# Kernel optimization log

Measured on AMD Instinct MI355X. Metric: run time of the kernel, lower is better.

The kernel has to match this reference:

```python
import jax, jax.numpy as jnp
import numpy as np

DIM = 3072
NUM_HEADS = 24
HEAD_DIM = 128
INNER = NUM_HEADS * HEAD_DIM
EPS = 1e-5


def _layernorm(x, eps=EPS):
    # affine-free LayerNorm over the last (head_dim) axis
    mu = jnp.mean(x, axis=-1, keepdims=True)
    var = jnp.mean(jnp.square(x - mu), axis=-1, keepdims=True)
    return (x - mu) * jax.lax.rsqrt(var + eps)


def _rope_interleaved(x, cos, sin):
    # x: (B, S_img, H, D); cos/sin: (S_img, D//2). Non-neox (interleaved) style.
    x1 = x[..., 0::2]
    x2 = x[..., 1::2]
    c = cos[None, :, None, :]
    s = sin[None, :, None, :]
    o1 = x1 * c - x2 * s
    o2 = x2 * c + x1 * s
    return jnp.stack([o1, o2], axis=-1).reshape(x.shape)


def setup_inputs() -> dict:
    key = jax.random.key(0)
    ks = jax.random.split(key, 8)
    B, S_txt, S_img = 1, 256, 2048
    hidden_states = jax.random.normal(ks[0], (B, S_img, DIM), dtype=jnp.float32)
    encoder_hidden_states = jax.random.normal(ks[1], (B, S_txt, DIM), dtype=jnp.float32)
    cos = jax.random.uniform(ks[2], (S_img, HEAD_DIM // 2), dtype=jnp.float32)
    sin = jax.random.uniform(ks[3], (S_img, HEAD_DIM // 2), dtype=jnp.float32)
    Wqkv = jax.random.normal(ks[4], (DIM, 3 * INNER), dtype=jnp.float32) * (DIM ** -0.5)
    bqkv = jnp.zeros((3 * INNER,), dtype=jnp.float32)
    Wout = jax.random.normal(ks[5], (INNER, DIM), dtype=jnp.float32) * (INNER ** -0.5)
    bout = jnp.zeros((DIM,), dtype=jnp.float32)
    return {
        "hidden_states": hidden_states,
        "encoder_hidden_states": encoder_hidden_states,
        "cos": cos,
        "sin": sin,
        "Wqkv": Wqkv,
        "bqkv": bqkv,
        "Wout": Wout,
        "bout": bout,
        "text_seq_length": 256,
    }


def reference(hidden_states, encoder_hidden_states, cos, sin, Wqkv, bqkv, Wout, bout, text_seq_length):
    T = text_seq_length
    x = jnp.concatenate([encoder_hidden_states, hidden_states], axis=1)  # (B, S, dim)
    B, S, _ = x.shape
    qkv = x @ Wqkv + bqkv  # (B, S, 3*inner)
    q, k, v = jnp.split(qkv, 3, axis=-1)
    q = q.reshape(B, S, NUM_HEADS, HEAD_DIM)
    k = k.reshape(B, S, NUM_HEADS, HEAD_DIM)
    v = v.reshape(B, S, NUM_HEADS, HEAD_DIM)
    q = _layernorm(q)
    k = _layernorm(k)
    # partial RoPE: only on image-token slice
    q = jnp.concatenate([q[:, :T], _rope_interleaved(q[:, T:], cos, sin)], axis=1)
    k = jnp.concatenate([k[:, :T], _rope_interleaved(k[:, T:], cos, sin)], axis=1)
    scale = 1.0 / (HEAD_DIM ** 0.5)
    scores = jnp.einsum("bqhd,bkhd->bhqk", q, k) * scale
    probs = jax.nn.softmax(scores, axis=-1)
    out = jnp.einsum("bhqk,bkhd->bqhd", probs, v)
    out = out.reshape(B, S, INNER)
    out = out @ Wout + bout
    encoder_out = out[:, :T, :]
    hidden_out = out[:, T:, :]
    return (hidden_out, encoder_out)
```

## Files before the change

### kernel.cpp

```cpp
#include <hip/hip_runtime.h>

#define DIMC 3072
#define NH 24
#define HD 128
#define QKV_N 9216
#define S_TXT 256
#define S_IMG 2048
#define S_TOT 2304

typedef _Float16 f16x8 __attribute__((ext_vector_type(8)));
typedef _Float16 f16x4 __attribute__((ext_vector_type(4)));
typedef _Float16 f16x2 __attribute__((ext_vector_type(2)));
typedef float f32x4 __attribute__((ext_vector_type(4)));

#define MFMA(A, B, C) __builtin_amdgcn_mfma_f32_16x16x32_f16(A, B, C, 0, 0, 0)

#define QSCALE (0.08838834764831845f * 1.4426950408889634f)

__device__ __forceinline__ void gl2lds16(const _Float16* g, _Float16* l) {
    __builtin_amdgcn_global_load_lds(
        (const __attribute__((address_space(1))) unsigned int*)g,
        (__attribute__((address_space(3))) unsigned int*)l,
        16, 0, 0);
}

__global__ __launch_bounds__(256) void prep(
    const float* __restrict__ enc, const float* __restrict__ hid,
    const float* __restrict__ Wqkv, const float* __restrict__ Wout,
    _Float16* __restrict__ xh, _Float16* __restrict__ Wth,
    _Float16* __restrict__ W2h)
{
    __shared__ float T[64][68];
    const int bid = blockIdx.x;
    const int t = threadIdx.x;

    if (bid < S_TOT) {
        const int s = bid;
        const float* src = (s < S_TXT) ? enc + (size_t)s * DIMC
                                       : hid + (size_t)(s - S_TXT) * DIMC;
#pragma unroll
        for (int it = 0; it < 3; ++it) {
            const int i = (it * 256 + t) * 4;
            float4 v = *(const float4*)(src + i);
            f16x4 hv;
            hv.x = (_Float16)v.x; hv.y = (_Float16)v.y;
            hv.z = (_Float16)v.z; hv.w = (_Float16)v.w;
            *(f16x4*)(xh + (size_t)s * DIMC + i) = hv;
        }
        return;
    }

    const float* W;
    _Float16* Th;
    int n0, k0, ldw;
    if (bid < S_TOT + 144 * 48) {
        const int b2 = bid - S_TOT;
        W = Wqkv; Th = Wth; ldw = QKV_N;
        n0 = (b2 % 144) * 64; k0 = (b2 / 144) * 64;
    } else {
        const int b2 = bid - S_TOT - 144 * 48;
        W = Wout; Th = W2h; ldw = DIMC;
        n0 = (b2 % 48) * 64; k0 = (b2 / 48) * 64;
    }
    {
        const int r = t >> 2, c4 = (t & 3) * 16;
#pragma unroll
        for (int j = 0; j < 4; ++j) {
            float4 v = *(const float4*)(W + (size_t)(k0 + r) * ldw + n0 + c4 + j * 4);
            *(float4*)&T[r][c4 + j * 4] = v;
        }
    }
    __syncthreads();
    const int nr = t >> 2, kp = (t & 3) * 16;
    f16x8 hv0, hv1;
#pragma unroll
    for (int j = 0; j < 8; ++j) hv0[j] = (_Float16)T[kp + j][nr];
#pragma unroll
    for (int j = 0; j < 8; ++j) hv1[j] = (_Float16)T[kp + 8 + j][nr];
    _Float16* dh = Th + (size_t)(n0 + nr) * DIMC + k0 + kp;
    *(f16x8*)(dh) = hv0; *(f16x8*)(dh + 8) = hv1;
}

#define GEMM_DB_PRE()                                                         \
    const int cpx = (int)gridDim.x >> 3;                                      \
    const int wgid = (blockIdx.x & 7) * cpx + (blockIdx.x >> 3);              \
    const int bm = (wgid % 18) * 128;                                         \
    const int bn = (wgid / 18) * 128;                                         \
    const int tid = threadIdx.x;                                              \
    const int l = tid & 63, w = tid >> 6;                                     \
    const int wr = w >> 1, wc = w & 1;                                        \
    const int lr = l & 15, g = l >> 4;                                        \
    const int row0 = w * 16 + (l >> 2);                                       \
    const int swz = (((l & 3) ^ ((row0 >> 1) & 3)) * 8);                      \
    const _Float16* gA0 = Ah + (size_t)(bm + row0) * DIMC + swz;              \
    const _Float16* gA1 = Ah + (size_t)(bm + 64 + row0) * DIMC + swz;         \
    const _Float16* gB0 = Bh + (size_t)(bn + row0) * DIMC + swz;              \
    const _Float16* gB1 = Bh + (size_t)(bn + 64 + row0) * DIMC + swz;         \
    int aoff[4], boff[4];                                                     \
    _Pragma("unroll")                                                         \
    for (int i = 0; i < 4; ++i) {                                             \
        const int ra = wr * 64 + i * 16 + lr;                                 \
        const int rb = wc * 64 + i * 16 + lr;                                 \
        aoff[i] = ra * 32 + ((g ^ ((ra >> 1) & 3)) * 8);                      \
        boff[i] = rb * 32 + ((g ^ ((rb >> 1) & 3)) * 8);                      \
    }

#define GEMM_STAGE(dd, k0) do {                                               \
    gl2lds16(gA0 + (k0), &Ash[dd][(w * 16) * 32]);                            \
    gl2lds16(gA1 + (k0), &Ash[dd][(64 + w * 16) * 32]);                       \
    gl2lds16(gB0 + (k0), &Bsh[dd][(w * 16) * 32]);                            \
    gl2lds16(gB1 + (k0), &Bsh[dd][(64 + w * 16) * 32]);                       \
} while (0)

#define GEMM_DB_LOOP()                                                        \
    f32x4 acc[4][4] = {};                                                     \
    GEMM_STAGE(0, 0);                                                         \
    __syncthreads();                                                          \
    for (int T = 0; T < DIMC / 32; ++T) {                                     \
        const int d = T & 1;                                                  \
        if (T + 1 < DIMC / 32) GEMM_STAGE(d ^ 1, (T + 1) * 32);               \
        f16x8 bhf[4];                                                         \
        _Pragma("unroll")                                                     \
        for (int ni = 0; ni < 4; ++ni)                                        \
            bhf[ni] = *(const f16x8*)&Bsh[d][boff[ni]];                       \
        __builtin_amdgcn_s_setprio(1);                                        \
        _Pragma("unroll")                                                     \
        for (int mi = 0; mi < 4; ++mi) {                                      \
            f16x8 ahf = *(const f16x8*)&Ash[d][aoff[mi]];                     \
            _Pragma("unroll")                                                 \
            for (int ni = 0; ni < 4; ++ni)                                    \
                acc[mi][ni] = MFMA(ahf, bhf[ni], acc[mi][ni]);                \
        }                                                                     \
        __builtin_amdgcn_s_setprio(0);                                        \
        __syncthreads();                                                      \
    }

__global__ __launch_bounds__(256) void gemm_qkv(
    const _Float16* __restrict__ Ah, const _Float16* __restrict__ Bh,
    const float* __restrict__ bias,
    _Float16* __restrict__ Qh, _Float16* __restrict__ Kh,
    _Float16* __restrict__ Vt)
{
    __shared__ __attribute__((aligned(16))) _Float16 Ash[2][128 * 32];
    __shared__ __attribute__((aligned(16))) _Float16 Bsh[2][128 * 32];
    GEMM_DB_PRE()
    GEMM_DB_LOOP()

    const int nb = bn >> 7;
    const int typ = nb / NH;
    const int h = nb % NH;

    if (typ == 2) {
#pragma unroll
        for (int mi = 0; mi < 4; ++mi) {
            const int sbase = bm + wr * 64 + mi * 16 + g * 4;
#pragma unroll
            for (int ni = 0; ni < 4; ++ni) {
                const int col = wc * 64 + ni * 16 + lr;
                const float bv = bias[bn + col];
                f16x4 vv;
                vv.x = (_Float16)(acc[mi][ni][0] + bv);
                vv.y = (_Float16)(acc[mi][ni][1] + bv);
                vv.z = (_Float16)(acc[mi][ni][2] + bv);
                vv.w = (_Float16)(acc[mi][ni][3] + bv);
                *(f16x4*)&Vt[((size_t)h * HD + col) * S_TOT + sbase] = vv;
            }
        }
    } else {
        _Float16* dst = (typ ? Kh : Qh) + (size_t)h * S_TOT * HD;
#pragma unroll
        for (int mi = 0; mi < 4; ++mi)
#pragma unroll
            for (int ni = 0; ni < 4; ++ni) {
                const int col = wc * 64 + ni * 16 + lr;
                const float bv = bias[bn + col];
#pragma unroll
                for (int e = 0; e < 4; ++e) {
                    const int r = bm + wr * 64 + mi * 16 + g * 4 + e;
                    dst[(size_t)r * HD + col] = (_Float16)(acc[mi][ni][e] + bv);
                }
            }
    }
}

__global__ __launch_bounds__(256) void gemm_out(
    const _Float16* __restrict__ Ah, const _Float16* __restrict__ Bh,
    const float* __restrict__ bias, float* __restrict__ C)
{
    __shared__ __attribute__((aligned(16))) _Float16 Ash[2][128 * 32];
    __shared__ __attribute__((aligned(16))) _Float16 Bsh[2][128 * 32];
    GEMM_DB_PRE()
    GEMM_DB_LOOP()

#pragma unroll
    for (int mi = 0; mi < 4; ++mi)
#pragma unroll
        for (int ni = 0; ni < 4; ++ni) {
            const int cl = bn + wc * 64 + ni * 16 + lr;
            const float bv = bias[cl];
#pragma unroll
            for (int e = 0; e < 4; ++e) {
                const int r = bm + wr * 64 + mi * 16 + g * 4 + e;
                const int gr = (r < S_TXT) ? (S_IMG + r) : (r - S_TXT);
                C[(size_t)gr * DIMC + cl] = acc[mi][ni][e] + bv;
            }
        }
}

__global__ __launch_bounds__(256) void ln_rope_inplace(
    _Float16* __restrict__ Qh, _Float16* __restrict__ Kh,
    const float* __restrict__ cost, const float* __restrict__ sint)
{
    const int wave = threadIdx.x >> 6;
    const int lane = threadIdx.x & 63;
    const int task = blockIdx.x * 4 + wave;
    const int s = task / 48;
    const int rem = task % 48;
    const int qk = rem / 24;
    const int h = rem % 24;

    _Float16* p = (qk ? Kh : Qh) + ((size_t)h * S_TOT + s) * HD + lane * 2;
    f16x2 xv = *(const f16x2*)p;
    float x0 = (float)xv.x, x1 = (float)xv.y;

    float sum = x0 + x1;
    float sq = x0 * x0 + x1 * x1;
#pragma unroll
    for (int off = 1; off < 64; off <<= 1) {
        sum += __shfl_xor(sum, off, 64);
        sq  += __shfl_xor(sq, off, 64);
    }
    const float mu = sum * (1.0f / 128.0f);
    const float var = sq * (1.0f / 128.0f) - mu * mu;
    const float rstd = rsqrtf(var + 1e-5f);
    float y0 = (x0 - mu) * rstd;
    float y1 = (x1 - mu) * rstd;

    if (s >= S_TXT) {
        const int ip = s - S_TXT;
        const float c = cost[ip * 64 + lane];
        const float sn = sint[ip * 64 + lane];
        const float o0 = y0 * c - y1 * sn;
        const float o1 = y1 * c + y0 * sn;
        y0 = o0; y1 = o1;
    }
    if (qk == 0) { y0 *= QSCALE; y1 *= QSCALE; }

    f16x2 hv; hv.x = (_Float16)y0; hv.y = (_Float16)y1;
    *(f16x2*)p = hv;
}

__global__ __launch_bounds__(512) void attn_mfma(
    const _Float16* __restrict__ Qg, const _Float16* __restrict__ Kg,
    const _Float16* __restrict__ Vg, _Float16* __restrict__ aoh)
{
    __shared__ __attribute__((aligned(16))) _Float16 Ksh[4 * 64 * 32];
    __shared__ __attribute__((aligned(16))) _Float16 Vsh[128 * 64];
    __shared__ __attribute__((aligned(16))) _Float16 Pah[8 * 16 * 64];

    const int wgid = ((int)blockIdx.x & 7) * 54 + ((int)blockIdx.x >> 3);
    const int h = wgid / 18;
    const int q0 = (wgid % 18) * 128;
    const int tid = threadIdx.x;
    const int w = tid >> 6, l = tid & 63;
    const int lr = l & 15, g = l >> 4;

    const int qrow = q0 + w * 16 + lr;
    const _Float16* qb = Qg + ((size_t)h * S_TOT + qrow) * HD + g * 8;
    f16x8 qh[4];
#pragma unroll
    for (int db = 0; db < 4; ++db)
        qh[db] = *(const f16x8*)(qb + db * 32);

    f32x4 o[8] = {};
    float mrow = -3.0e38f, lrow = 0.0f;

    const int kxr = (lr >> 1) & 3;
    const int px  = lr & 7;
    int ksl[4];
#pragma unroll
    for (int db = 0; db < 4; ++db) ksl[db] = (g ^ kxr ^ db) * 8;
    const int vs0 = (g ^ px) * 8;
    const int vs1 = ((4 + g) ^ px) * 8;

    const int kkv = tid >> 3, kd = tid & 7;
    const int kdb = kd >> 1, kg0 = (kd & 1) * 2;
    const int kx = (kkv >> 1) & 3;
    const int kbase = kdb * 2048 + kkv * 32;
    const int vd = tid >> 2, vh = tid & 3;
    const int vx = vd & 7;
    const int vbase = vd * 64;
    const int vg0 = vh * 2;
    const _Float16* gK = Kg + ((size_t)h * S_TOT + kkv) * HD + kd * 16;
    const _Float16* gV = Vg + ((size_t)h * HD + vd) * S_TOT + vh * 16;

    uint4 rK0, rK1, rV0, rV1;
#define LOADKV(kv0) { \
    rK0 = *(const uint4*)(gK + (size_t)(kv0) * HD);     rK1 = *(const uint4*)(gK + (size_t)(kv0) * HD + 8); \
    rV0 = *(const uint4*)(gV + (kv0));                  rV1 = *(const uint4*)(gV + (kv0) + 8); }

    LOADKV(0);

    for (int kb = 0; kb < S_TOT / 64; ++kb) {
        __syncthreads();
        *(uint4*)&Ksh[kbase + (((kg0 + 0) ^ kx ^ kdb) * 8)] = rK0;
        *(uint4*)&Ksh[kbase + (((kg0 + 1) ^ kx ^ kdb) * 8)] = rK1;
        *(uint4*)&Vsh[vbase + (((vg0 + 0) ^ vx) * 8)] = rV0;
        *(uint4*)&Vsh[vbase + (((vg0 + 1) ^ vx) * 8)] = rV1;
        __syncthreads();
        if (kb + 1 < S_TOT / 64) LOADKV((kb + 1) * 64);

        f32x4 sT[4] = {};
        __builtin_amdgcn_s_setprio(1);
#pragma unroll
        for (int db = 0; db < 4; ++db)
#pragma unroll
            for (int mf = 0; mf < 4; ++mf) {
                f16x8 kf = *(const f16x8*)&Ksh[db * 2048 + (mf * 16 + lr) * 32 + ksl[db]];
                sT[mf] = MFMA(kf, qh[db], sT[mf]);
            }
        __builtin_amdgcn_s_setprio(0);

        float pm = -3.0e38f;
#pragma unroll
        for (int mf = 0; mf < 4; ++mf)
#pragma unroll
            for (int e = 0; e < 4; ++e)
                pm = fmaxf(pm, sT[mf][e]);
        pm = fmaxf(pm, __shfl_xor(pm, 16, 64));
        pm = fmaxf(pm, __shfl_xor(pm, 32, 64));

        if (__any(pm > mrow + 11.0f)) {
            const float mnew = fmaxf(mrow, pm);
            const float alpha = exp2f(mrow - mnew);
            lrow *= alpha;
            mrow = mnew;
            const float a0 = __shfl(alpha, g * 4 + 0, 64);
            const float a1 = __shfl(alpha, g * 4 + 1, 64);
            const float a2 = __shfl(alpha, g * 4 + 2, 64);
            const float a3 = __shfl(alpha, g * 4 + 3, 64);
#pragma unroll
            for (int df = 0; df < 8; ++df) {
                o[df][0] *= a0; o[df][1] *= a1; o[df][2] *= a2; o[df][3] *= a3;
            }
        }

        float rs = 0.0f;
        float ex_[4][4];
#pragma unroll
        for (int mf = 0; mf < 4; ++mf)
#pragma unroll
            for (int e = 0; e < 4; ++e) {
                const float pv = exp2f(sT[mf][e] - mrow);
                ex_[mf][e] = pv;
                rs += pv;
            }
        rs += __shfl_xor(rs, 16, 64);
        rs += __shfl_xor(rs, 32, 64);
        lrow += rs;

        {
            const int pbase = w * 1024 + lr * 64;
#pragma unroll
            for (int mf = 0; mf < 4; ++mf) {
                const int slot = ((mf * 2 + (g >> 1)) ^ px) * 8 + (g & 1) * 4;
                f16x2 t0; t0.x = (_Float16)ex_[mf][0]; t0.y = (_Float16)ex_[mf][1];
                f16x2 t1; t1.x = (_Float16)ex_[mf][2]; t1.y = (_Float16)ex_[mf][3];
                *(f16x2*)&Pah[pbase + slot]     = t0;
                *(f16x2*)&Pah[pbase + slot + 2] = t1;
            }
        }

        f16x8 pa0 = *(const f16x8*)&Pah[w * 1024 + lr * 64 + vs0];
        f16x8 pa1 = *(const f16x8*)&Pah[w * 1024 + lr * 64 + vs1];
        __builtin_amdgcn_s_setprio(1);
#pragma unroll
        for (int df = 0; df < 8; ++df) {
            f16x8 vf0 = *(const f16x8*)&Vsh[(df * 16 + lr) * 64 + vs0];
            f16x8 vf1 = *(const f16x8*)&Vsh[(df * 16 + lr) * 64 + vs1];
            o[df] = MFMA(pa0, vf0, o[df]);
            o[df] = MFMA(pa1, vf1, o[df]);
        }
        __builtin_amdgcn_s_setprio(0);
    }
#undef LOADKV

    const float inv = 1.0f / lrow;
    const float b0 = __shfl(inv, g * 4 + 0, 64);
    const float b1 = __shfl(inv, g * 4 + 1, 64);
    const float b2 = __shfl(inv, g * 4 + 2, 64);
    const float b3 = __shfl(inv, g * 4 + 3, 64);
    const float bb[4] = {b0, b1, b2, b3};
#pragma unroll
    for (int df = 0; df < 8; ++df)
#pragma unroll
        for (int e = 0; e < 4; ++e) {
            const int r = q0 + w * 16 + g * 4 + e;
            aoh[(size_t)r * DIMC + h * HD + df * 16 + lr] = (_Float16)(o[df][e] * bb[e]);
        }
}

extern "C" void kernel_launch(void* const* d_in, const int* in_sizes, int n_in,
                              void* d_out, int out_size, void* d_ws, size_t ws_size,
                              hipStream_t stream)
{
    const float* hid  = (const float*)d_in[0];
    const float* enc  = (const float*)d_in[1];
    const float* cost = (const float*)d_in[2];
    const float* sint = (const float*)d_in[3];
    const float* Wqkv = (const float*)d_in[4];
    const float* bqkv = (const float*)d_in[5];
    const float* Wout = (const float*)d_in[6];
    const float* bout = (const float*)d_in[7];
    float* out = (float*)d_out;

    char* ws = (char*)d_ws;
    _Float16* Qh  = (_Float16*)(ws + 0);
    _Float16* Kh  = (_Float16*)(ws + 14155776);
    _Float16* Vth = (_Float16*)(ws + 28311552);
    _Float16* aoh = (_Float16*)(ws + 42467328);
    _Float16* xh  = (_Float16*)(ws + 56623104);
    _Float16* Wth = (_Float16*)(ws + 70778880);
    _Float16* W2h = (_Float16*)(ws + 127401984);

    prep<<<S_TOT + 144 * 48 + 48 * 48, 256, 0, stream>>>(
        enc, hid, Wqkv, Wout, xh, Wth, W2h);
    gemm_qkv<<<18 * 72, 256, 0, stream>>>(xh, Wth, bqkv, Qh, Kh, Vth);
    ln_rope_inplace<<<(S_TOT * 48) / 4, 256, 0, stream>>>(Qh, Kh, cost, sint);
    attn_mfma<<<432, 512, 0, stream>>>(Qh, Kh, Vth, aoh);
    gemm_out<<<18 * 24, 256, 0, stream>>>(aoh, W2h, bout, out);
}
```

Baseline: 457.4 us.

## Single-buffer GEMM LDS staging and give each attention wave two query tiles

The GEMM kernels drop the double-buffered LDS pipeline and the setprio hints. They now load each K-slice synchronously and sync before compute, with the per-wave load rows remapped. The attention kernel halves its block size to 4 waves, and each wave processes 32 query rows as two 16-row tiles. This reuses every K/V fragment read from LDS across two MFMA streams and halves the waves contending for the K/V tiles. The cost is higher register pressure and lost load/compute overlap in the GEMMs, which risks stalls on global-to-LDS latency.

```diff
diff --git a/kernel.cpp b/kernel.cpp
--- a/kernel.cpp
+++ b/kernel.cpp
@@ -81,7 +81,7 @@
     *(f16x8*)(dh) = hv0; *(f16x8*)(dh + 8) = hv1;
 }
 
-#define GEMM_DB_PRE()                                                         \
+#define GEMM_PRE()                                                            \
     const int cpx = (int)gridDim.x >> 3;                                      \
     const int wgid = (blockIdx.x & 7) * cpx + (blockIdx.x >> 3);              \
     const int bm = (wgid % 18) * 128;                                         \
@@ -90,12 +90,18 @@
     const int l = tid & 63, w = tid >> 6;                                     \
     const int wr = w >> 1, wc = w & 1;                                        \
     const int lr = l & 15, g = l >> 4;                                        \
-    const int row0 = w * 16 + (l >> 2);                                       \
-    const int swz = (((l & 3) ^ ((row0 >> 1) & 3)) * 8);                      \
-    const _Float16* gA0 = Ah + (size_t)(bm + row0) * DIMC + swz;              \
-    const _Float16* gA1 = Ah + (size_t)(bm + 64 + row0) * DIMC + swz;         \
-    const _Float16* gB0 = Bh + (size_t)(bn + row0) * DIMC + swz;              \
-    const _Float16* gB1 = Bh + (size_t)(bn + 64 + row0) * DIMC + swz;         \
+    const int srow0 = w * 32 + (l >> 2);                                      \
+    const int srow1 = srow0 + 16;                                             \
+    const int skp0 = (((l & 3) ^ ((srow0 >> 1) & 3)) * 8);                    \
+    const int skp1 = (((l & 3) ^ ((srow1 >> 1) & 3)) * 8);                    \
+    const _Float16* gA0 = Ah + (size_t)(bm + srow0) * DIMC + skp0;            \
+    const _Float16* gA1 = Ah + (size_t)(bm + srow1) * DIMC + skp1;            \
+    const _Float16* gB0 = Bh + (size_t)(bn + srow0) * DIMC + skp0;            \
+    const _Float16* gB1 = Bh + (size_t)(bn + srow1) * DIMC + skp1;            \
+    _Float16* lA0 = &Ash[(w * 32) * 32];                                      \
+    _Float16* lA1 = &Ash[(w * 32 + 16) * 32];                                 \
+    _Float16* lB0 = &Bsh[(w * 32) * 32];                                      \
+    _Float16* lB1 = &Bsh[(w * 32 + 16) * 32];                                 \
     int aoff[4], boff[4];                                                     \
     _Pragma("unroll")                                                         \
     for (int i = 0; i < 4; ++i) {                                             \
@@ -103,35 +109,27 @@
         const int rb = wc * 64 + i * 16 + lr;                                 \
         aoff[i] = ra * 32 + ((g ^ ((ra >> 1) & 3)) * 8);                      \
         boff[i] = rb * 32 + ((g ^ ((rb >> 1) & 3)) * 8);                      \
-    }
-
-#define GEMM_STAGE(dd, k0) do {                                               \
-    gl2lds16(gA0 + (k0), &Ash[dd][(w * 16) * 32]);                            \
-    gl2lds16(gA1 + (k0), &Ash[dd][(64 + w * 16) * 32]);                       \
-    gl2lds16(gB0 + (k0), &Bsh[dd][(w * 16) * 32]);                            \
-    gl2lds16(gB1 + (k0), &Bsh[dd][(64 + w * 16) * 32]);                       \
-} while (0)
-
-#define GEMM_DB_LOOP()                                                        \
-    f32x4 acc[4][4] = {};                                                     \
-    GEMM_STAGE(0, 0);                                                         \
-    __syncthreads();                                                          \
-    for (int T = 0; T < DIMC / 32; ++T) {                                     \
-        const int d = T & 1;                                                  \
-        if (T + 1 < DIMC / 32) GEMM_STAGE(d ^ 1, (T + 1) * 32);               \
+    }                                                                         \
+    f32x4 acc[4][4] = {};
+
+#define GEMM_LOOP()                                                           \
+    for (int k0 = 0; k0 < DIMC; k0 += 32) {                                   \
+        gl2lds16(gA0 + k0, lA0);                                              \
+        gl2lds16(gA1 + k0, lA1);                                              \
+        gl2lds16(gB0 + k0, lB0);                                              \
+        gl2lds16(gB1 + k0, lB1);                                              \
+        __syncthreads();                                                      \
         f16x8 bhf[4];                                                         \
         _Pragma("unroll")                                                     \
         for (int ni = 0; ni < 4; ++ni)                                        \
-            bhf[ni] = *(const f16x8*)&Bsh[d][boff[ni]];                       \
-        __builtin_amdgcn_s_setprio(1);                                        \
+            bhf[ni] = *(const f16x8*)&Bsh[boff[ni]];                          \
         _Pragma("unroll")                                                     \
         for (int mi = 0; mi < 4; ++mi) {                                      \
-            f16x8 ahf = *(const f16x8*)&Ash[d][aoff[mi]];                     \
+            f16x8 ahf = *(const f16x8*)&Ash[aoff[mi]];                        \
             _Pragma("unroll")                                                 \
             for (int ni = 0; ni < 4; ++ni)                                    \
                 acc[mi][ni] = MFMA(ahf, bhf[ni], acc[mi][ni]);                \
         }                                                                     \
-        __builtin_amdgcn_s_setprio(0);                                        \
         __syncthreads();                                                      \
     }
 
@@ -141,10 +139,10 @@
     _Float16* __restrict__ Qh, _Float16* __restrict__ Kh,
     _Float16* __restrict__ Vt)
 {
-    __shared__ __attribute__((aligned(16))) _Float16 Ash[2][128 * 32];
-    __shared__ __attribute__((aligned(16))) _Float16 Bsh[2][128 * 32];
-    GEMM_DB_PRE()
-    GEMM_DB_LOOP()
+    __shared__ __attribute__((aligned(16))) _Float16 Ash[128 * 32];
+    __shared__ __attribute__((aligned(16))) _Float16 Bsh[128 * 32];
+    GEMM_PRE()
+    GEMM_LOOP()
 
     const int nb = bn >> 7;
     const int typ = nb / NH;
@@ -187,10 +185,10 @@
     const _Float16* __restrict__ Ah, const _Float16* __restrict__ Bh,
     const float* __restrict__ bias, float* __restrict__ C)
 {
-    __shared__ __attribute__((aligned(16))) _Float16 Ash[2][128 * 32];
-    __shared__ __attribute__((aligned(16))) _Float16 Bsh[2][128 * 32];
-    GEMM_DB_PRE()
-    GEMM_DB_LOOP()
+    __shared__ __attribute__((aligned(16))) _Float16 Ash[128 * 32];
+    __shared__ __attribute__((aligned(16))) _Float16 Bsh[128 * 32];
+    GEMM_PRE()
+    GEMM_LOOP()
 
 #pragma unroll
     for (int mi = 0; mi < 4; ++mi)
@@ -250,13 +248,13 @@
     *(f16x2*)p = hv;
 }
 
-__global__ __launch_bounds__(512) void attn_mfma(
+__global__ __launch_bounds__(256) void attn_mfma(
     const _Float16* __restrict__ Qg, const _Float16* __restrict__ Kg,
     const _Float16* __restrict__ Vg, _Float16* __restrict__ aoh)
 {
     __shared__ __attribute__((aligned(16))) _Float16 Ksh[4 * 64 * 32];
     __shared__ __attribute__((aligned(16))) _Float16 Vsh[128 * 64];
-    __shared__ __attribute__((aligned(16))) _Float16 Pah[8 * 16 * 64];
+    __shared__ __attribute__((aligned(16))) _Float16 Pah[4 * 32 * 64];
 
     const int wgid = ((int)blockIdx.x & 7) * 54 + ((int)blockIdx.x >> 3);
     const int h = wgid / 18;
@@ -265,15 +263,19 @@
     const int w = tid >> 6, l = tid & 63;
     const int lr = l & 15, g = l >> 4;
 
-    const int qrow = q0 + w * 16 + lr;
-    const _Float16* qb = Qg + ((size_t)h * S_TOT + qrow) * HD + g * 8;
-    f16x8 qh[4];
-#pragma unroll
-    for (int db = 0; db < 4; ++db)
-        qh[db] = *(const f16x8*)(qb + db * 32);
-
-    f32x4 o[8] = {};
-    float mrow = -3.0e38f, lrow = 0.0f;
+    const int qrow = q0 + w * 32 + lr;
+    const _Float16* qb0 = Qg + ((size_t)h * S_TOT + qrow) * HD + g * 8;
+    const _Float16* qb1 = qb0 + (size_t)16 * HD;
+    f16x8 qh0[4], qh1[4];
+#pragma unroll
+    for (int db = 0; db < 4; ++db) {
+        qh0[db] = *(const f16x8*)(qb0 + db * 32);
+        qh1[db] = *(const f16x8*)(qb1 + db * 32);
+    }
+
+    f32x4 o0[8] = {}, o1[8] = {};
+    float m0 = -3.0e38f, l0s = 0.0f;
+    float m1 = -3.0e38f, l1s = 0.0f;
 
     const int kxr = (lr >> 1) & 3;
     const int px  = lr & 7;
@@ -283,120 +285,158 @@
     const int vs0 = (g ^ px) * 8;
     const int vs1 = ((4 + g) ^ px) * 8;
 
-    const int kkv = tid >> 3, kd = tid & 7;
-    const int kdb = kd >> 1, kg0 = (kd & 1) * 2;
+    const int kkv = tid >> 2, kdb = tid & 3;
     const int kx = (kkv >> 1) & 3;
     const int kbase = kdb * 2048 + kkv * 32;
-    const int vd = tid >> 2, vh = tid & 3;
+    const int vd = tid >> 1;
+    const int vbase = vd * 64;
     const int vx = vd & 7;
-    const int vbase = vd * 64;
-    const int vg0 = vh * 2;
-    const _Float16* gK = Kg + ((size_t)h * S_TOT + kkv) * HD + kd * 16;
-    const _Float16* gV = Vg + ((size_t)h * HD + vd) * S_TOT + vh * 16;
-
-    uint4 rK0, rK1, rV0, rV1;
+    const int vg0 = (tid & 1) * 4;
+    const _Float16* gK = Kg + ((size_t)h * S_TOT + kkv) * HD + kdb * 32;
+    const _Float16* gV = Vg + ((size_t)h * HD + vd) * S_TOT + (tid & 1) * 32;
+
+    uint4 rK0, rK1, rK2, rK3, rV0, rV1, rV2, rV3;
 #define LOADKV(kv0) { \
-    rK0 = *(const uint4*)(gK + (size_t)(kv0) * HD);     rK1 = *(const uint4*)(gK + (size_t)(kv0) * HD + 8); \
-    rV0 = *(const uint4*)(gV + (kv0));                  rV1 = *(const uint4*)(gV + (kv0) + 8); }
+    rK0 = *(const uint4*)(gK + (size_t)(kv0) * HD);      rK1 = *(const uint4*)(gK + (size_t)(kv0) * HD + 8); \
+    rK2 = *(const uint4*)(gK + (size_t)(kv0) * HD + 16); rK3 = *(const uint4*)(gK + (size_t)(kv0) * HD + 24); \
+    rV0 = *(const uint4*)(gV + (kv0));      rV1 = *(const uint4*)(gV + (kv0) + 8); \
+    rV2 = *(const uint4*)(gV + (kv0) + 16); rV3 = *(const uint4*)(gV + (kv0) + 24); }
 
     LOADKV(0);
 
     for (int kb = 0; kb < S_TOT / 64; ++kb) {
         __syncthreads();
-        *(uint4*)&Ksh[kbase + (((kg0 + 0) ^ kx ^ kdb) * 8)] = rK0;
-        *(uint4*)&Ksh[kbase + (((kg0 + 1) ^ kx ^ kdb) * 8)] = rK1;
+        *(uint4*)&Ksh[kbase + ((0 ^ kx ^ kdb) * 8)] = rK0;
+        *(uint4*)&Ksh[kbase + ((1 ^ kx ^ kdb) * 8)] = rK1;
+        *(uint4*)&Ksh[kbase + ((2 ^ kx ^ kdb) * 8)] = rK2;
+        *(uint4*)&Ksh[kbase + ((3 ^ kx ^ kdb) * 8)] = rK3;
         *(uint4*)&Vsh[vbase + (((vg0 + 0) ^ vx) * 8)] = rV0;
         *(uint4*)&Vsh[vbase + (((vg0 + 1) ^ vx) * 8)] = rV1;
+        *(uint4*)&Vsh[vbase + (((vg0 + 2) ^ vx) * 8)] = rV2;
+        *(uint4*)&Vsh[vbase + (((vg0 + 3) ^ vx) * 8)] = rV3;
         __syncthreads();
         if (kb + 1 < S_TOT / 64) LOADKV((kb + 1) * 64);
 
-        f32x4 sT[4] = {};
+        f32x4 sT0[4] = {}, sT1[4] = {};
         __builtin_amdgcn_s_setprio(1);
 #pragma unroll
         for (int db = 0; db < 4; ++db)
 #pragma unroll
             for (int mf = 0; mf < 4; ++mf) {
                 f16x8 kf = *(const f16x8*)&Ksh[db * 2048 + (mf * 16 + lr) * 32 + ksl[db]];
-                sT[mf] = MFMA(kf, qh[db], sT[mf]);
+                sT0[mf] = MFMA(kf, qh0[db], sT0[mf]);
+                sT1[mf] = MFMA(kf, qh1[db], sT1[mf]);
             }
         __builtin_amdgcn_s_setprio(0);
 
-        float pm = -3.0e38f;
+        float pm0 = -3.0e38f, pm1 = -3.0e38f;
 #pragma unroll
         for (int mf = 0; mf < 4; ++mf)
 #pragma unroll
-            for (int e = 0; e < 4; ++e)
-                pm = fmaxf(pm, sT[mf][e]);
-        pm = fmaxf(pm, __shfl_xor(pm, 16, 64));
-        pm = fmaxf(pm, __shfl_xor(pm, 32, 64));
-
-        if (__any(pm > mrow + 11.0f)) {
-            const float mnew = fmaxf(mrow, pm);
-            const float alpha = exp2f(mrow - mnew);
-            lrow *= alpha;
-            mrow = mnew;
-            const float a0 = __shfl(alpha, g * 4 + 0, 64);
-            const float a1 = __shfl(alpha, g * 4 + 1, 64);
-            const float a2 = __shfl(alpha, g * 4 + 2, 64);
-            const float a3 = __shfl(alpha, g * 4 + 3, 64);
+            for (int e = 0; e < 4; ++e) {
+                pm0 = fmaxf(pm0, sT0[mf][e]);
+                pm1 = fmaxf(pm1, sT1[mf][e]);
+            }
+        pm0 = fmaxf(pm0, __shfl_xor(pm0, 16, 64));
+        pm0 = fmaxf(pm0, __shfl_xor(pm0, 32, 64));
+        pm1 = fmaxf(pm1, __shfl_xor(pm1, 16, 64));
+        pm1 = fmaxf(pm1, __shfl_xor(pm1, 32, 64));
+
+        if (__any((pm0 > m0 + 11.0f) || (pm1 > m1 + 11.0f))) {
+            const float mn0 = fmaxf(m0, pm0);
+            const float al0 = exp2f(m0 - mn0);
+            l0s *= al0; m0 = mn0;
+            const float mn1 = fmaxf(m1, pm1);
+            const float al1 = exp2f(m1 - mn1);
+            l1s *= al1; m1 = mn1;
+            const float a0 = __shfl(al0, g * 4 + 0, 64);
+            const float a1 = __shfl(al0, g * 4 + 1, 64);
+            const float a2 = __shfl(al0, g * 4 + 2, 64);
+            const float a3 = __shfl(al0, g * 4 + 3, 64);
+            const float b0 = __shfl(al1, g * 4 + 0, 64);
+            const float b1 = __shfl(al1, g * 4 + 1, 64);
+            const float b2 = __shfl(al1, g * 4 + 2, 64);
+            const float b3 = __shfl(al1, g * 4 + 3, 64);
 #pragma unroll
             for (int df = 0; df < 8; ++df) {
-                o[df][0] *= a0; o[df][1] *= a1; o[df][2] *= a2; o[df][3] *= a3;
-            }
-        }
-
-        float rs = 0.0f;
-        float ex_[4][4];
+                o0[df][0] *= a0; o0[df][1] *= a1; o0[df][2] *= a2; o0[df][3] *= a3;
+                o1[df][0] *= b0; o1[df][1] *= b1; o1[df][2] *= b2; o1[df][3] *= b3;
+            }
+        }
+
+        float rs0 = 0.0f, rs1 = 0.0f;
+        float ex0[4][4], ex1[4][4];
 #pragma unroll
         for (int mf = 0; mf < 4; ++mf)
 #pragma unroll
             for (int e = 0; e < 4; ++e) {
-                const float pv = exp2f(sT[mf][e] - mrow);
-                ex_[mf][e] = pv;
-                rs += pv;
-            }
-        rs += __shfl_xor(rs, 16, 64);
-        rs += __shfl_xor(rs, 32, 64);
-        lrow += rs;
+                const float p0 = exp2f(sT0[mf][e] - m0);
+                const float p1 = exp2f(sT1[mf][e] - m1);
+                ex0[mf][e] = p0; rs0 += p0;
+                ex1[mf][e] = p1; rs1 += p1;
+            }
+        rs0 += __shfl_xor(rs0, 16, 64);
+        rs0 += __shfl_xor(rs0, 32, 64);
+        rs1 += __shfl_xor(rs1, 16, 64);
+        rs1 += __shfl_xor(rs1, 32, 64);
+        l0s += rs0;
+        l1s += rs1;
 
         {
-            const int pbase = w * 1024 + lr * 64;
+            const int pb0 = w * 2048 + lr * 64;
+            const int pb1 = w * 2048 + (16 + lr) * 64;
 #pragma unroll
             for (int mf = 0; mf < 4; ++mf) {
                 const int slot = ((mf * 2 + (g >> 1)) ^ px) * 8 + (g & 1) * 4;
-                f16x2 t0; t0.x = (_Float16)ex_[mf][0]; t0.y = (_Float16)ex_[mf][1];
-                f16x2 t1; t1.x = (_Float16)ex_[mf][2]; t1.y = (_Float16)ex_[mf][3];
-                *(f16x2*)&Pah[pbase + slot]     = t0;
-                *(f16x2*)&Pah[pbase + slot + 2] = t1;
-            }
-        }
-
-        f16x8 pa0 = *(const f16x8*)&Pah[w * 1024 + lr * 64 + vs0];
-        f16x8 pa1 = *(const f16x8*)&Pah[w * 1024 + lr * 64 + vs1];
+                f16x2 t0; t0.x = (_Float16)ex0[mf][0]; t0.y = (_Float16)ex0[mf][1];
+                f16x2 t1; t1.x = (_Float16)ex0[mf][2]; t1.y = (_Float16)ex0[mf][3];
+                f16x2 u0; u0.x = (_Float16)ex1[mf][0]; u0.y = (_Float16)ex1[mf][1];
+                f16x2 u1; u1.x = (_Float16)ex1[mf][2]; u1.y = (_Float16)ex1[mf][3];
+                *(f16x2*)&Pah[pb0 + slot]     = t0;
+                *(f16x2*)&Pah[pb0 + slot + 2] = t1;
+                *(f16x2*)&Pah[pb1 + slot]     = u0;
+                *(f16x2*)&Pah[pb1 + slot + 2] = u1;
+            }
+        }
+
+        f16x8 pa0a = *(const f16x8*)&Pah[w * 2048 + lr * 64 + vs0];
+        f16x8 pa0b = *(const f16x8*)&Pah[w * 2048 + lr * 64 + vs1];
+        f16x8 pa1a = *(const f16x8*)&Pah[w * 2048 + (16 + lr) * 64 + vs0];
+        f16x8 pa1b = *(const f16x8*)&Pah[w * 2048 + (16 + lr) * 64 + vs1];
         __builtin_amdgcn_s_setprio(1);
 #pragma unroll
         for (int df = 0; df < 8; ++df) {
             f16x8 vf0 = *(const f16x8*)&Vsh[(df * 16 + lr) * 64 + vs0];
             f16x8 vf1 = *(const f16x8*)&Vsh[(df * 16 + lr) * 64 + vs1];
-            o[df] = MFMA(pa0, vf0, o[df]);
-            o[df] = MFMA(pa1, vf1, o[df]);
+            o0[df] = MFMA(pa0a, vf0, o0[df]);
+            o0[df] = MFMA(pa0b, vf1, o0[df]);
+            o1[df] = MFMA(pa1a, vf0, o1[df]);
+            o1[df] = MFMA(pa1b, vf1, o1[df]);
         }
         __builtin_amdgcn_s_setprio(0);
     }
 #undef LOADKV
 
-    const float inv = 1.0f / lrow;
-    const float b0 = __shfl(inv, g * 4 + 0, 64);
-    const float b1 = __shfl(inv, g * 4 + 1, 64);
-    const float b2 = __shfl(inv, g * 4 + 2, 64);
-    const float b3 = __shfl(inv, g * 4 + 3, 64);
-    const float bb[4] = {b0, b1, b2, b3};
+    const float i0 = 1.0f / l0s;
+    const float i1 = 1.0f / l1s;
+    const float c0 = __shfl(i0, g * 4 + 0, 64);
+    const float c1 = __shfl(i0, g * 4 + 1, 64);
+    const float c2 = __shfl(i0, g * 4 + 2, 64);
+    const float c3 = __shfl(i0, g * 4 + 3, 64);
+    const float d0 = __shfl(i1, g * 4 + 0, 64);
+    const float d1 = __shfl(i1, g * 4 + 1, 64);
+    const float d2 = __shfl(i1, g * 4 + 2, 64);
+    const float d3 = __shfl(i1, g * 4 + 3, 64);
+    const float cc[4] = {c0, c1, c2, c3};
+    const float dd[4] = {d0, d1, d2, d3};
 #pragma unroll
     for (int df = 0; df < 8; ++df)
 #pragma unroll
         for (int e = 0; e < 4; ++e) {
-            const int r = q0 + w * 16 + g * 4 + e;
-            aoh[(size_t)r * DIMC + h * HD + df * 16 + lr] = (_Float16)(o[df][e] * bb[e]);
+            const int r0 = q0 + w * 32 + g * 4 + e;
+            const int col = h * HD + df * 16 + lr;
+            aoh[(size_t)r0 * DIMC + col] = (_Float16)(o0[df][e] * cc[e]);
+            aoh[(size_t)(r0 + 16) * DIMC + col] = (_Float16)(o1[df][e] * dd[e]);
         }
 }
 
@@ -427,6 +467,6 @@
         enc, hid, Wqkv, Wout, xh, Wth, W2h);
     gemm_qkv<<<18 * 72, 256, 0, stream>>>(xh, Wth, bqkv, Qh, Kh, Vth);
     ln_rope_inplace<<<(S_TOT * 48) / 4, 256, 0, stream>>>(Qh, Kh, cost, sint);
-    attn_mfma<<<432, 512, 0, stream>>>(Qh, Kh, Vth, aoh);
+    attn_mfma<<<432, 256, 0, stream>>>(Qh, Kh, Vth, aoh);
     gemm_out<<<18 * 24, 256, 0, stream>>>(aoh, W2h, bout, out);
 }
```

Result: no change. 449.1 us (-1.8%).
